# Optimization experiments

Measured on AMD Instinct MI355X. Metric: run time of the kernel, lower is better.

Reference implementation:

```python
import jax, jax.numpy as jnp
import numpy as np

EMBED_DIM = 1024
NUM_HEADS = 16
HEAD_DIM = EMBED_DIM // NUM_HEADS


def setup_inputs() -> dict:
    key = jax.random.key(0)
    k_x, k_qkv, k_proj, k_pb = jax.random.split(key, 4)
    B, N = 8, 1024
    s = 1.0 / np.sqrt(EMBED_DIM)
    return {
        "x": jax.random.normal(k_x, (B, N, EMBED_DIM), dtype=jnp.float32),
        # qkv: Linear(embed_dim -> 3*all_head_dim), bias=False
        "w_qkv": jax.random.uniform(k_qkv, (EMBED_DIM, 3 * EMBED_DIM), dtype=jnp.float32, minval=-s, maxval=s),
        # proj: Linear(all_head_dim -> embed_dim), with bias
        "w_proj": jax.random.uniform(k_proj, (EMBED_DIM, EMBED_DIM), dtype=jnp.float32, minval=-s, maxval=s),
        "b_proj": jax.random.uniform(k_pb, (EMBED_DIM,), dtype=jnp.float32, minval=-s, maxval=s),
    }


def reference(x, w_qkv, w_proj, b_proj):
    B, N, _ = x.shape
    scale = HEAD_DIM ** -0.5
    qkv = jnp.einsum("bnd,de->bne", x, w_qkv)  # [B, N, 3*D]
    q, k, v = jnp.split(qkv, 3, axis=-1)
    # reshape to heads: [B, H, N, hd]
    def heads(t):
        return t.reshape(B, N, NUM_HEADS, HEAD_DIM).transpose(0, 2, 1, 3)
    q, k, v = heads(q), heads(k), heads(v)
    attn = jnp.einsum("bhqd,bhkd->bhqk", q, k) * scale
    attn = jax.nn.softmax(attn, axis=-1)
    out = jnp.einsum("bhqk,bhkd->bhqd", attn, v)
    out = out.transpose(0, 2, 1, 3).reshape(B, N, NUM_HEADS * HEAD_DIM)
    return jnp.einsum("bnd,de->bne", out, w_proj) + b_proj
```

## Files before the change

kernel.cpp:

```cpp
#include <hip/hip_runtime.h>
#include <hip/hip_bf16.h>
#include <stdint.h>

typedef __hip_bfloat16 bf16;
typedef __attribute__((ext_vector_type(8))) __bf16 bf16x8;
typedef __attribute__((ext_vector_type(4))) float f32x4;

__device__ __forceinline__ bf16x8 load8bf(const bf16* p) {
    return __builtin_bit_cast(bf16x8, *(const int4*)p);
}

__device__ __forceinline__ void async16(const bf16* g, bf16* l) {
    __builtin_amdgcn_global_load_lds((const __attribute__((address_space(1))) void*)g,
                                     (__attribute__((address_space(3))) void*)l, 16, 0, 0);
}

__global__ __launch_bounds__(256) void cast_x_kernel(const float* __restrict__ in,
                                                     bf16* __restrict__ out, int n4) {
    int i = blockIdx.x * 256 + threadIdx.x;
    if (i >= n4) return;
    float4 v = ((const float4*)in)[i];
    ushort4 o;
    o.x = __builtin_bit_cast(unsigned short, __float2bfloat16(v.x));
    o.y = __builtin_bit_cast(unsigned short, __float2bfloat16(v.y));
    o.z = __builtin_bit_cast(unsigned short, __float2bfloat16(v.z));
    o.w = __builtin_bit_cast(unsigned short, __float2bfloat16(v.w));
    ((ushort4*)out)[i] = o;
}

__global__ __launch_bounds__(256) void transpose_cast(const float* __restrict__ in,
                                                      bf16* __restrict__ out, int R, int C) {
    __shared__ float t[32][33];
    int c0 = blockIdx.x * 32, r0 = blockIdx.y * 32;
    int tx = threadIdx.x, ty = threadIdx.y;
#pragma unroll
    for (int j = 0; j < 32; j += 8)
        t[ty + j][tx] = in[(size_t)(r0 + ty + j) * C + c0 + tx];
    __syncthreads();
#pragma unroll
    for (int j = 0; j < 32; j += 8)
        out[(size_t)(c0 + ty + j) * R + r0 + tx] = __float2bfloat16(t[tx][ty + j]);
}

template <int MODE>
__global__ __launch_bounds__(256, 3) void gemm_bt(
    const bf16* __restrict__ A, const bf16* __restrict__ Bt,
    int M, int N, int K,
    bf16* __restrict__ qo, bf16* __restrict__ ko, bf16* __restrict__ vto,
    float* __restrict__ out, const float* __restrict__ bias) {
    __shared__ __align__(16) bf16 A0[128 * 32];
    __shared__ __align__(16) bf16 B0[128 * 32];
    __shared__ __align__(16) bf16 A1[128 * 32];
    __shared__ __align__(16) bf16 B1[128 * 32];
    __shared__ __align__(16) bf16 A2[128 * 32];
    __shared__ __align__(16) bf16 B2[128 * 32];
    const int tid = threadIdx.x;
    const int l = tid & 63, wid = tid >> 6;
    const int lo = l & 15, hi = l >> 4;
    const int wm = wid >> 1, wn = wid & 1;
    const int m0 = blockIdx.x * 128, n0 = blockIdx.y * 128;
    const int tsr = tid >> 2;
    const int tsc = tid & 3;
    const int csw = ((tsc ^ (tsr & 3)) * 8);
    const int cl  = tsc * 8;
    const int colr = ((hi ^ (lo & 3)) * 8);

    f32x4 acc[4][4];
#pragma unroll
    for (int i = 0; i < 4; ++i)
#pragma unroll
        for (int j = 0; j < 4; ++j) acc[i][j] = f32x4{0.f, 0.f, 0.f, 0.f};

#define STAGE32(AD, BD, KT)                                                           \
    {                                                                                 \
        async16(A + (size_t)(m0 + tsr) * K + (KT) * 32 + csw, (AD) + tsr * 32 + cl);  \
        async16(A + (size_t)(m0 + 64 + tsr) * K + (KT) * 32 + csw,                    \
                (AD) + (64 + tsr) * 32 + cl);                                         \
        async16(Bt + (size_t)(n0 + tsr) * K + (KT) * 32 + csw, (BD) + tsr * 32 + cl); \
        async16(Bt + (size_t)(n0 + 64 + tsr) * K + (KT) * 32 + csw,                   \
                (BD) + (64 + tsr) * 32 + cl);                                         \
    }

#define KB(AC, BC, AS, BS, KT, STG, WAITASM)                                          \
    {                                                                                 \
        __builtin_amdgcn_s_barrier();           \
        __builtin_amdgcn_sched_barrier(0);       \
        if (STG) STAGE32(AS, BS, (KT) + 2)                                            \
        __builtin_amdgcn_sched_barrier(0);          \
        asm volatile(WAITASM ::: "memory");                                           \
        __builtin_amdgcn_s_barrier();            \
        __builtin_amdgcn_sched_barrier(0);       \
        bf16x8 af[4], bf_[4];                                                         \
        _Pragma("unroll") for (int mt = 0; mt < 4; ++mt)                              \
            af[mt] = load8bf((AC) + (wm * 64 + mt * 16 + lo) * 32 + colr);            \
        _Pragma("unroll") for (int nt = 0; nt < 4; ++nt)                              \
            bf_[nt] = load8bf((BC) + (wn * 64 + nt * 16 + lo) * 32 + colr);           \
        _Pragma("unroll") for (int mt = 0; mt < 4; ++mt)                              \
            _Pragma("unroll") for (int nt = 0; nt < 4; ++nt)                          \
                acc[mt][nt] = __builtin_amdgcn_mfma_f32_16x16x32_bf16(                \
                    af[mt], bf_[nt], acc[mt][nt], 0, 0, 0);                           \
    }

    const int nkt = K / 32;
    STAGE32(A0, B0, 0)
    STAGE32(A1, B1, 1)
    for (int kt = 0; kt + 5 < nkt; kt += 3) {
        KB(A0, B0, A2, B2, kt, true, "s_waitcnt vmcnt(8)")
        KB(A1, B1, A0, B0, kt + 1, true, "s_waitcnt vmcnt(8)")
        KB(A2, B2, A1, B1, kt + 2, true, "s_waitcnt vmcnt(8)")
    }
    KB(A0, B0, A2, B2, 27, true, "s_waitcnt vmcnt(8)")
    KB(A1, B1, A0, B0, 28, true, "s_waitcnt vmcnt(8)")
    KB(A2, B2, A1, B1, 29, true, "s_waitcnt vmcnt(8)")
    KB(A0, B0, A2, B2, 30, false, "s_waitcnt vmcnt(4)")
    KB(A1, B1, A2, B2, 31, false, "s_waitcnt vmcnt(0)")
#undef KB
#undef STAGE32

#pragma unroll
    for (int mt = 0; mt < 4; ++mt)
#pragma unroll
        for (int nt = 0; nt < 4; ++nt)
#pragma unroll
            for (int r = 0; r < 4; ++r) {
                int row = m0 + wm * 64 + mt * 16 + hi * 4 + r;
                int col = n0 + wn * 64 + nt * 16 + lo;
                float v = acc[mt][nt][r];
                if (MODE == 0) {
                    if (col < 1024) {
                        qo[(size_t)row * 1024 + col] = __float2bfloat16(v * 0.125f);
                    } else if (col < 2048) {
                        ko[(size_t)row * 1024 + (col - 1024)] = __float2bfloat16(v);
                    } else {
                        int c = col - 2048;
                        vto[((size_t)(row >> 10) * 1024 + c) * 1024 + (row & 1023)] = __float2bfloat16(v);
                    }
                } else {
                    out[(size_t)row * N + col] = v + bias[col];
                }
            }
}

__global__ __launch_bounds__(256, 3) void flash_attn(
    const bf16* __restrict__ q,
    const bf16* __restrict__ kin,
    const bf16* __restrict__ vt,
    bf16* __restrict__ out)
{
    __shared__ __align__(16) bf16 Kl0[64 * 64];
    __shared__ __align__(16) bf16 Vl0[64 * 64];
    __shared__ __align__(16) bf16 Kl1[64 * 64];
    __shared__ __align__(16) bf16 Vl1[64 * 64];
    __shared__ __align__(16) bf16 Pl[4 * 32 * 72];
    const int tid = threadIdx.x;
    const int l = tid & 63, w = tid >> 6;
    const int lo = l & 15, hi = l >> 4;
    const int bid = (blockIdx.x & 7) * 128 + (blockIdx.x >> 3);
    const int qt = bid & 7, h = (bid >> 3) & 15, b = bid >> 7;
    const int ts_r = tid >> 3;
    const int ts_c = tid & 7;
    const int ts_csw = (ts_c ^ (ts_r & 7)) * 8;
    const int ts_lds = tid * 8;

    const bf16* kbase = kin + (size_t)(b * 1024) * 1024 + h * 64;
    const bf16* vbase = vt + (size_t)(b * 1024 + h * 64) * 1024;

#define STAGE_KV(KD, VD, KT)                                                          \
    {                                                                                 \
        async16(kbase + (size_t)((KT) * 64 + ts_r) * 1024 + ts_csw, (KD) + ts_lds);   \
        async16(kbase + (size_t)((KT) * 64 + 32 + ts_r) * 1024 + ts_csw,              \
                (KD) + 2048 + ts_lds);                                                \
        async16(vbase + (size_t)ts_r * 1024 + (KT) * 64 + ts_csw, (VD) + ts_lds);     \
        async16(vbase + (size_t)(32 + ts_r) * 1024 + (KT) * 64 + ts_csw,              \
                (VD) + 2048 + ts_lds);                                                \
    }

    bf16x8 qf[2][2];
#pragma unroll
    for (int mt = 0; mt < 2; ++mt)
#pragma unroll
        for (int ks = 0; ks < 2; ++ks) {
            int tok = qt * 128 + w * 32 + mt * 16 + lo;
            qf[mt][ks] = load8bf(q + (size_t)(b * 1024 + tok) * 1024 + h * 64 + ks * 32 + hi * 8);
        }

    float lsum[2][4];
    f32x4 oacc[2][4];
#pragma unroll
    for (int mt = 0; mt < 2; ++mt)
#pragma unroll
        for (int r = 0; r < 4; ++r) lsum[mt][r] = 0.f;
#pragma unroll
    for (int mt = 0; mt < 2; ++mt)
#pragma unroll
        for (int nt = 0; nt < 4; ++nt) oacc[mt][nt] = f32x4{0.f, 0.f, 0.f, 0.f};

    STAGE_KV(Kl0, Vl0, 0)
    __syncthreads();

#define FA_ITER(KC, VC, KN, VN, KT, STG)                                              \
    {                                                                                 \
        if (STG) { STAGE_KV(KN, VN, (KT) + 1) }                                       \
        __builtin_amdgcn_sched_barrier(0);                                            \
        f32x4 s[2][4];                                                                \
        _Pragma("unroll") for (int mt = 0; mt < 2; ++mt)                              \
            _Pragma("unroll") for (int nt = 0; nt < 4; ++nt)                          \
                s[mt][nt] = f32x4{0.f, 0.f, 0.f, 0.f};                                \
        _Pragma("unroll") for (int ks = 0; ks < 2; ++ks) {                            \
            bf16x8 kf[4];                                                             \
            _Pragma("unroll") for (int nt = 0; nt < 4; ++nt) {                        \
                int kr = nt * 16 + lo;                                                \
                kf[nt] = load8bf((KC) + kr * 64 + ((ks * 32 + hi * 8) ^ ((kr & 7) * 8))); \
            }                                                                         \
            _Pragma("unroll") for (int mt = 0; mt < 2; ++mt)                          \
                _Pragma("unroll") for (int nt = 0; nt < 4; ++nt)                      \
                    s[mt][nt] = __builtin_amdgcn_mfma_f32_16x16x32_bf16(              \
                        qf[mt][ks], kf[nt], s[mt][nt], 0, 0, 0);                      \
        }                                                                             \
        _Pragma("unroll") for (int mt = 0; mt < 2; ++mt)                              \
            _Pragma("unroll") for (int nt = 0; nt < 4; ++nt)                          \
                _Pragma("unroll") for (int r = 0; r < 4; ++r) {                       \
                    float p = __expf(s[mt][nt][r]);                                   \
                    lsum[mt][r] += p;                                                 \
                    Pl[(w * 32 + mt * 16 + hi * 4 + r) * 72 + nt * 16 + lo] =         \
                        __float2bfloat16(p);                                          \
                }                                                                     \
        _Pragma("unroll") for (int ks = 0; ks < 2; ++ks) {                            \
            bf16x8 vf[4], pf[2];                                                      \
            _Pragma("unroll") for (int nt = 0; nt < 4; ++nt) {                        \
                int vr = nt * 16 + lo;                                                \
                vf[nt] = load8bf((VC) + vr * 64 + ((ks * 32 + hi * 8) ^ ((vr & 7) * 8))); \
            }                                                                         \
            _Pragma("unroll") for (int mt = 0; mt < 2; ++mt)                          \
                pf[mt] = load8bf(Pl + (w * 32 + mt * 16 + lo) * 72 + ks * 32 + hi * 8); \
            _Pragma("unroll") for (int mt = 0; mt < 2; ++mt)                          \
                _Pragma("unroll") for (int nt = 0; nt < 4; ++nt)                      \
                    oacc[mt][nt] = __builtin_amdgcn_mfma_f32_16x16x32_bf16(           \
                        pf[mt], vf[nt], oacc[mt][nt], 0, 0, 0);                       \
        }                                                                             \
        __syncthreads();                                                              \
    }

    for (int kt = 0; kt < 16; kt += 2) {
        FA_ITER(Kl0, Vl0, Kl1, Vl1, kt, true)
        FA_ITER(Kl1, Vl1, Kl0, Vl0, kt + 1, (kt + 2 < 16))
    }
#undef FA_ITER
#undef STAGE_KV

#pragma unroll
    for (int mt = 0; mt < 2; ++mt)
#pragma unroll
        for (int r = 0; r < 4; ++r) {
#pragma unroll
            for (int off = 1; off < 16; off <<= 1)
                lsum[mt][r] += __shfl_xor(lsum[mt][r], off);
        }

#pragma unroll
    for (int mt = 0; mt < 2; ++mt)
#pragma unroll
        for (int nt = 0; nt < 4; ++nt)
#pragma unroll
            for (int r = 0; r < 4; ++r) {
                int tok = qt * 128 + w * 32 + mt * 16 + hi * 4 + r;
                int d = nt * 16 + lo;
                out[(size_t)(b * 1024 + tok) * 1024 + h * 64 + d] =
                    __float2bfloat16(oacc[mt][nt][r] / lsum[mt][r]);
            }
}

extern "C" void kernel_launch(void* const* d_in, const int* in_sizes, int n_in,
                              void* d_out, int out_size, void* d_ws, size_t ws_size,
                              hipStream_t stream) {
    const float* x      = (const float*)d_in[0];
    const float* w_qkv  = (const float*)d_in[1];
    const float* w_proj = (const float*)d_in[2];
    const float* b_proj = (const float*)d_in[3];
    float* out = (float*)d_out;

    char* ws = (char*)d_ws;
    bf16* xb     = (bf16*)(ws);
    bf16* wqkvT  = (bf16*)(ws + (16ull << 20));
    bf16* wprojT = (bf16*)(ws + (22ull << 20));
    bf16* qb     = (bf16*)(ws + (24ull << 20));
    bf16* kb     = (bf16*)(ws + (40ull << 20));
    bf16* vtb    = (bf16*)(ws + (56ull << 20));
    bf16* attn   = xb;

    cast_x_kernel<<<8192, 256, 0, stream>>>(x, xb, 2 * 1024 * 1024);
    transpose_cast<<<dim3(96, 32), dim3(32, 8), 0, stream>>>(w_qkv, wqkvT, 1024, 3072);
    transpose_cast<<<dim3(32, 32), dim3(32, 8), 0, stream>>>(w_proj, wprojT, 1024, 1024);
    gemm_bt<0><<<dim3(64, 24), 256, 0, stream>>>(xb, wqkvT, 8192, 3072, 1024,
                                                 qb, kb, vtb, nullptr, nullptr);
    flash_attn<<<1024, 256, 0, stream>>>(qb, kb, vtb, attn);
    gemm_bt<1><<<dim3(64, 8), 256, 0, stream>>>(attn, wprojT, 8192, 1024, 1024,
                                                nullptr, nullptr, nullptr, out, b_proj);
}
```

Before: 166.0 us.

## Switch GEMM to double-buffered LDS pipeline with higher occupancy target

Replaces the three-stage LDS prefetch pipeline in the bf16 GEMM with a two-buffer ping-pong loop. It uses __syncthreads instead of explicit vmcnt waits and split barriers. Dropping the third buffer cuts LDS use, and launch bounds are raised from 3 to 4 blocks per CU. The LDS XOR swizzle now keys on (row>>1)&3 in both the store and read paths. The trade is less load/compute overlap per block in exchange for more resident blocks.

```diff
diff --git a/kernel.cpp b/kernel.cpp
--- a/kernel.cpp
+++ b/kernel.cpp
@@ -43,7 +43,7 @@
 }
 
 template <int MODE>
-__global__ __launch_bounds__(256, 3) void gemm_bt(
+__global__ __launch_bounds__(256, 4) void gemm_bt(
     const bf16* __restrict__ A, const bf16* __restrict__ Bt,
     int M, int N, int K,
     bf16* __restrict__ qo, bf16* __restrict__ ko, bf16* __restrict__ vto,
@@ -52,8 +52,6 @@
     __shared__ __align__(16) bf16 B0[128 * 32];
     __shared__ __align__(16) bf16 A1[128 * 32];
     __shared__ __align__(16) bf16 B1[128 * 32];
-    __shared__ __align__(16) bf16 A2[128 * 32];
-    __shared__ __align__(16) bf16 B2[128 * 32];
     const int tid = threadIdx.x;
     const int l = tid & 63, wid = tid >> 6;
     const int lo = l & 15, hi = l >> 4;
@@ -61,9 +59,8 @@
     const int m0 = blockIdx.x * 128, n0 = blockIdx.y * 128;
     const int tsr = tid >> 2;
     const int tsc = tid & 3;
-    const int csw = ((tsc ^ (tsr & 3)) * 8);
+    const int csw = (tsc ^ ((tsr >> 1) & 3)) * 8;
     const int cl  = tsc * 8;
-    const int colr = ((hi ^ (lo & 3)) * 8);
 
     f32x4 acc[4][4];
 #pragma unroll
@@ -81,20 +78,20 @@
                 (BD) + (64 + tsr) * 32 + cl);                                         \
     }
 
-#define KB(AC, BC, AS, BS, KT, STG, WAITASM)                                          \
-    {                                                                                 \
-        __builtin_amdgcn_s_barrier();           \
-        __builtin_amdgcn_sched_barrier(0);       \
-        if (STG) STAGE32(AS, BS, (KT) + 2)                                            \
-        __builtin_amdgcn_sched_barrier(0);          \
-        asm volatile(WAITASM ::: "memory");                                           \
-        __builtin_amdgcn_s_barrier();            \
-        __builtin_amdgcn_sched_barrier(0);       \
+#define KB32(AC, BC, AS, BS, KT, STG)                                                 \
+    {                                                                                 \
+        __syncthreads();                                                              \
+        if (STG) STAGE32(AS, BS, (KT) + 1)                                            \
+        __builtin_amdgcn_sched_barrier(0);                                            \
         bf16x8 af[4], bf_[4];                                                         \
-        _Pragma("unroll") for (int mt = 0; mt < 4; ++mt)                              \
-            af[mt] = load8bf((AC) + (wm * 64 + mt * 16 + lo) * 32 + colr);            \
-        _Pragma("unroll") for (int nt = 0; nt < 4; ++nt)                              \
-            bf_[nt] = load8bf((BC) + (wn * 64 + nt * 16 + lo) * 32 + colr);           \
+        _Pragma("unroll") for (int mt = 0; mt < 4; ++mt) {                            \
+            int ar = wm * 64 + mt * 16 + lo;                                          \
+            af[mt] = load8bf((AC) + ar * 32 + ((hi ^ ((ar >> 1) & 3)) * 8));          \
+        }                                                                             \
+        _Pragma("unroll") for (int nt = 0; nt < 4; ++nt) {                            \
+            int br = wn * 64 + nt * 16 + lo;                                          \
+            bf_[nt] = load8bf((BC) + br * 32 + ((hi ^ ((br >> 1) & 3)) * 8));         \
+        }                                                                             \
         _Pragma("unroll") for (int mt = 0; mt < 4; ++mt)                              \
             _Pragma("unroll") for (int nt = 0; nt < 4; ++nt)                          \
                 acc[mt][nt] = __builtin_amdgcn_mfma_f32_16x16x32_bf16(                \
@@ -103,18 +100,11 @@
 
     const int nkt = K / 32;
     STAGE32(A0, B0, 0)
-    STAGE32(A1, B1, 1)
-    for (int kt = 0; kt + 5 < nkt; kt += 3) {
-        KB(A0, B0, A2, B2, kt, true, "s_waitcnt vmcnt(8)")
-        KB(A1, B1, A0, B0, kt + 1, true, "s_waitcnt vmcnt(8)")
-        KB(A2, B2, A1, B1, kt + 2, true, "s_waitcnt vmcnt(8)")
-    }
-    KB(A0, B0, A2, B2, 27, true, "s_waitcnt vmcnt(8)")
-    KB(A1, B1, A0, B0, 28, true, "s_waitcnt vmcnt(8)")
-    KB(A2, B2, A1, B1, 29, true, "s_waitcnt vmcnt(8)")
-    KB(A0, B0, A2, B2, 30, false, "s_waitcnt vmcnt(4)")
-    KB(A1, B1, A2, B2, 31, false, "s_waitcnt vmcnt(0)")
-#undef KB
+    for (int kt = 0; kt < nkt; kt += 2) {
+        KB32(A0, B0, A1, B1, kt, true)
+        KB32(A1, B1, A0, B0, kt + 1, (kt + 2 < nkt))
+    }
+#undef KB32
 #undef STAGE32
 
 #pragma unroll
```

Result: no change. 165.0 us (-0.6%).
